# Performance work log

Measured on AMD Instinct MI355X. Metric: run time of the kernel, lower is better.

## Reference

```python
import jax, jax.numpy as jnp
import numpy as np

B, N = 64, 4096          # batch of diagrams, points per diagram
H, W = 64, 64            # persistence-image resolution
L, R = 5, 256            # num_landscapes, landscape resolution
EPS = 1e-8


def setup_inputs() -> dict:
    key = jax.random.key(0)
    k1, = jax.random.split(key, 1)
    u = jax.random.uniform(k1, (B, N, 2), dtype=jnp.float32)
    birth = u[..., 0] * 0.5                      # births in [0, 0.5]
    death = birth + u[..., 1] * 0.5 + 1e-3       # deaths > births, in range
    pairs = jnp.stack([birth, death], axis=-1)   # (B, N, 2)
    sigma = jnp.float32(0.1)                     # learned bandwidth (nn.Parameter)
    return {"pairs": pairs, "sigma": sigma}


def reference(pairs, sigma):
    # ---- Persistence image (batched, vectorized over points) ----
    grid_x = jnp.linspace(0.0, 1.0, W, dtype=pairs.dtype)   # birth axis
    grid_y = jnp.linspace(0.0, 1.0, H, dtype=pairs.dtype)   # persistence axis
    birth = pairs[..., 0]                 # (B, N)
    death = pairs[..., 1]                 # (B, N)
    pers = death - birth                  # (B, N)
    # normalization per config ranges (0,1): divide by (range + 1e-8)
    birth_n = birth / (1.0 + EPS)
    pers_n = pers / (1.0 + EPS)
    weights = pers                        # weight_fn == 'linear'
    inv2s2 = 1.0 / (2.0 * sigma * sigma)
    # separable Gaussian factors: (B, N, W) and (B, N, H)
    gx = jnp.exp(-(grid_x[None, None, :] - birth_n[..., None]) ** 2 * inv2s2)
    gy = jnp.exp(-(grid_y[None, None, :] - pers_n[..., None]) ** 2 * inv2s2)
    # sum_n wt_n * gy_n(h) * gx_n(w)  ->  (B, H, W)
    image = jnp.einsum('bnh,bnw->bhw', gy * weights[..., None], gx)
    image = image / (jnp.max(image, axis=(1, 2), keepdims=True) + EPS)

    # ---- Persistence landscapes ----
    min_b = jnp.min(birth, axis=1, keepdims=True)   # (B, 1)
    max_d = jnp.max(death, axis=1, keepdims=True)   # (B, 1)
    frac = jnp.linspace(0.0, 1.0, R, dtype=pairs.dtype)
    t = min_b + (max_d - min_b) * frac[None, :]     # (B, R)
    rising = jnp.clip(t[:, None, :] - birth[..., None], 0.0)   # (B, N, R)
    falling = jnp.clip(death[..., None] - t[:, None, :], 0.0)  # (B, N, R)
    tents = jnp.minimum(rising, falling)                        # (B, N, R)
    # descending sort over points + take top L == top_k over point axis
    top = jax.lax.top_k(jnp.swapaxes(tents, 1, 2), L)[0]        # (B, R, L)
    landscapes = jnp.swapaxes(top, 1, 2)                        # (B, L, R)
    return image, landscapes
```

## Files before the change

kernel.cpp:

```cpp
#include <hip/hip_runtime.h>
#include <math.h>


#define B_   64
#define N_   4096
#define HW_  64
#define RES_ 256
#define EPSF 1e-8f
#define KC_  8
#define CPB  512
#define LPC_ 8

typedef short short8v  __attribute__((ext_vector_type(8)));
typedef float float4v  __attribute__((ext_vector_type(4)));

__device__ __forceinline__ unsigned pk_bf(float a, float b) {
    unsigned ua = __float_as_uint(a), ub = __float_as_uint(b);
    return ((ua + 0x8000u) >> 16) | ((ub + 0x8000u) & 0xffff0000u);
}

#define INS5(v0, v1, v2, v3, v4, x)                       \
    {                                                     \
        float _p0 = v0, _p1 = v1, _p2 = v2, _p3 = v3;     \
        v0 = fmaxf(_p0, x);                               \
        v1 = __builtin_amdgcn_fmed3f(_p0, _p1, x);        \
        v2 = __builtin_amdgcn_fmed3f(_p1, _p2, x);        \
        v3 = __builtin_amdgcn_fmed3f(_p2, _p3, x);        \
        v4 = __builtin_amdgcn_fmed3f(_p3, v4, x);         \
    }

union SmemU {
    struct {
        unsigned short gy[64 * 72];
        unsigned short gx[64 * 72];
    } img;
    struct {
        float red[8];
    } land;
};

__global__ __launch_bounds__(256) void k_partial(const float* __restrict__ pairs,
                                                 const float* __restrict__ sigp,
                                                 float* __restrict__ part,
                                                 float* __restrict__ lp) {
    __shared__ SmemU sm;
    int tid = threadIdx.x;
    int l = tid & 63;
    int w = __builtin_amdgcn_readfirstlane(tid >> 6);
    int role = blockIdx.x & 1;
    int id   = blockIdx.x >> 1;

    if (role == 0) {
        int kc = id & 7, b = id >> 3;
        float sigma = sigp[0];
        float ncc2 = -(0.5f / (sigma * sigma)) * 1.4426950408889634f;

        int c = tid & 63;
        float xc = (float)c * (1.0f / 63.0f);

        float4v acc[4];
        #pragma unroll
        for (int c4 = 0; c4 < 4; ++c4) acc[c4] = (float4v){0.f, 0.f, 0.f, 0.f};

        int rowA = (w * 16 + (l & 15)) * 72 + (l >> 4) * 8;
        const float4* pb4 = (const float4*)(pairs + 2 * ((size_t)b * N_ + kc * CPB));

        for (int ch = 0; ch < CPB / 64; ++ch) {
            int p0 = ch * 32 + w * 8;
            unsigned gxp[8], gyp[8];
            #pragma unroll
            for (int jp = 0; jp < 8; ++jp) {
                float4 q = pb4[p0 + jp];
                float pe0 = q.y - q.x, pe1 = q.w - q.z;
                float dx0 = xc - q.x, dx1 = xc - q.z;
                float dy0 = xc - pe0, dy1 = xc - pe1;
                float ex0 = __builtin_amdgcn_exp2f(dx0 * dx0 * ncc2);
                float ex1 = __builtin_amdgcn_exp2f(dx1 * dx1 * ncc2);
                float ey0 = pe0 * __builtin_amdgcn_exp2f(dy0 * dy0 * ncc2);
                float ey1 = pe1 * __builtin_amdgcn_exp2f(dy1 * dy1 * ncc2);
                gxp[jp] = pk_bf(ex0, ex1);
                gyp[jp] = pk_bf(ey0, ey1);
            }
            __syncthreads();
            *(uint4*)&sm.img.gy[c * 72 + w * 16]     = *(uint4*)&gyp[0];
            *(uint4*)&sm.img.gy[c * 72 + w * 16 + 8] = *(uint4*)&gyp[4];
            *(uint4*)&sm.img.gx[c * 72 + w * 16]     = *(uint4*)&gxp[0];
            *(uint4*)&sm.img.gx[c * 72 + w * 16 + 8] = *(uint4*)&gxp[4];
            __syncthreads();
            #pragma unroll
            for (int ks = 0; ks < 2; ++ks) {
                short8v af = *(const short8v*)&sm.img.gy[rowA + ks * 32];
                #pragma unroll
                for (int c4 = 0; c4 < 4; ++c4) {
                    short8v bf = *(const short8v*)
                        &sm.img.gx[(c4 * 16 + (l & 15)) * 72 + ks * 32 + (l >> 4) * 8];
                    acc[c4] = __builtin_amdgcn_mfma_f32_16x16x32_bf16(af, bf, acc[c4], 0, 0, 0);
                }
            }
        }

        float* dst = part + (size_t)(b * KC_ + kc) * (HW_ * HW_);
        #pragma unroll
        for (int c4 = 0; c4 < 4; ++c4)
            #pragma unroll
            for (int reg = 0; reg < 4; ++reg) {
                int h = w * 16 + (l >> 4) * 4 + reg;
                int wv = c4 * 16 + (l & 15);
                dst[h * HW_ + wv] = acc[c4][reg];
            }
    } else {
        int pc = id & 7, b = id >> 3;

        const float4* pb4 = (const float4*)(pairs + 2 * (size_t)b * N_);
        float mn = 1e30f, mx = -1e30f;
        #pragma unroll
        for (int i = 0; i < 8; ++i) {
            float4 q = pb4[tid + i * 256];
            mn = fminf(mn, fminf(q.x, q.z));
            mx = fmaxf(mx, fmaxf(q.y, q.w));
        }
        #pragma unroll
        for (int off = 32; off > 0; off >>= 1) {
            mn = fminf(mn, __shfl_xor(mn, off, 64));
            mx = fmaxf(mx, __shfl_xor(mx, off, 64));
        }
        if ((tid & 63) == 0) { sm.land.red[w] = mn; sm.land.red[4 + w] = mx; }
        __syncthreads();
        float minb = fminf(fminf(sm.land.red[0], sm.land.red[1]),
                           fminf(sm.land.red[2], sm.land.red[3]));
        float maxd = fmaxf(fmaxf(sm.land.red[4], sm.land.red[5]),
                           fmaxf(sm.land.red[6], sm.land.red[7]));

        float sc = (maxd - minb) * (1.0f / 255.0f);
        float t  = minb + sc * (float)(w * 64 + l);
        float tlo_f = minb + sc * (float)(w * 64);
        float thi_f = minb + sc * (float)(w * 64 + 63);
        int itlo = __builtin_amdgcn_readfirstlane(__float_as_int(tlo_f));
        int ithi = __builtin_amdgcn_readfirstlane(__float_as_int(thi_f));

        float v0 = 0.f, v1 = 0.f, v2 = 0.f, v3 = 0.f, v4 = 0.f;
        const float4* pw = (const float4*)(pairs + 2 * ((size_t)b * N_ + pc * 512));
        #pragma unroll 2
        for (int p = 0; p < 256; ++p) {
            float4 q = pw[p];
            if (__float_as_int(q.y) > itlo && __float_as_int(q.x) < ithi) {
                float x = fminf(t - q.x, q.y - t);
                INS5(v0, v1, v2, v3, v4, x);
            }
            if (__float_as_int(q.w) > itlo && __float_as_int(q.z) < ithi) {
                float x = fminf(t - q.z, q.w - t);
                INS5(v0, v1, v2, v3, v4, x);
            }
        }

        float* dl = lp + ((size_t)((b * LPC_ + pc) * 4 + w)) * 320;
        dl[0 * 64 + l] = v0;
        dl[1 * 64 + l] = v1;
        dl[2 * 64 + l] = v2;
        dl[3 * 64 + l] = v3;
        dl[4 * 64 + l] = v4;
    }
}

__global__ __launch_bounds__(256) void k_finish(const float* __restrict__ part,
                                                const float* __restrict__ lp,
                                                float* __restrict__ out) {
    __shared__ float redf[4];
    int tid = threadIdx.x;
    if (blockIdx.x < 64) {
        int b = blockIdx.x;
        const float4* p0 = (const float4*)(part + (size_t)b * KC_ * (HW_ * HW_));
        float4 s[4];
        float m = 0.0f;
        #pragma unroll
        for (int i = 0; i < 4; ++i) {
            int pix4 = tid + i * 256;
            float4 v = p0[pix4];
            #pragma unroll
            for (int k2 = 1; k2 < KC_; ++k2) {
                float4 u = p0[(size_t)k2 * 1024 + pix4];
                v.x += u.x; v.y += u.y; v.z += u.z; v.w += u.w;
            }
            s[i] = v;
            m = fmaxf(m, fmaxf(fmaxf(v.x, v.y), fmaxf(v.z, v.w)));
        }
        #pragma unroll
        for (int off = 32; off > 0; off >>= 1) m = fmaxf(m, __shfl_xor(m, off, 64));
        if ((tid & 63) == 0) redf[tid >> 6] = m;
        __syncthreads();
        m = fmaxf(fmaxf(redf[0], redf[1]), fmaxf(redf[2], redf[3]));
        float inv = 1.0f / (m + EPSF);
        float4* od = (float4*)(out + (size_t)b * (HW_ * HW_));
        #pragma unroll
        for (int i = 0; i < 4; ++i) {
            float4 v = s[i];
            v.x *= inv; v.y *= inv; v.z *= inv; v.w *= inv;
            od[tid + i * 256] = v;
        }
    } else {
        int b = blockIdx.x - 64;
        int wq = tid >> 6, l = tid & 63;
        const float* lpb = lp + (size_t)b * (LPC_ * 4 * 320) + wq * 320 + l;
        float u0 = lpb[0 * 64], u1 = lpb[1 * 64], u2 = lpb[2 * 64],
              u3 = lpb[3 * 64], u4 = lpb[4 * 64];
        for (int p2 = 1; p2 < LPC_; ++p2) {
            const float* s2 = lpb + (size_t)p2 * 4 * 320;
            #pragma unroll
            for (int lvl = 0; lvl < 5; ++lvl) {
                float x = s2[lvl * 64];
                INS5(u0, u1, u2, u3, u4, x);
            }
        }
        float* o = out + (size_t)B_ * HW_ * HW_ + (size_t)b * (5 * RES_);
        o[tid]            = u0;
        o[RES_ + tid]     = u1;
        o[2 * RES_ + tid] = u2;
        o[3 * RES_ + tid] = u3;
        o[4 * RES_ + tid] = u4;
    }
}

extern "C" void kernel_launch(void* const* d_in, const int* in_sizes, int n_in,
                              void* d_out, int out_size, void* d_ws, size_t ws_size,
                              hipStream_t stream) {
    const float* pairs = (const float*)d_in[0];
    const float* sig   = (const float*)d_in[1];
    float* out = (float*)d_out;
    float* wsf = (float*)d_ws;

    float* part = wsf;
    float* lp   = part + (size_t)B_ * KC_ * HW_ * HW_;

    k_partial<<<1024, 256, 0, stream>>>(pairs, sig, part, lp);
    k_finish<<<128, 256, 0, stream>>>(part, lp, out);
}
```

Measured before the change: 105.0 us.

## Split partial work finer, precompute min/max in a separate kernel, drop landscape culling branch

Doubles the number of point chunks for both the image and landscape partial sums, giving 2048 blocks instead of 1024. The per-diagram min/max reduction moves out of every landscape block into a small dedicated kernel whose results are read from workspace. The per-point range-culling branch in the landscape insertion loop becomes straight-line code, unrolled by 4, to avoid divergence and branch overhead. The cost is an extra kernel launch, twice as many partial image buffers for the finish kernel to write and reduce, and doing all five median insertions for every point.

```diff
diff --git a/kernel.cpp b/kernel.cpp
--- a/kernel.cpp
+++ b/kernel.cpp
@@ -7,9 +7,9 @@
 #define HW_  64
 #define RES_ 256
 #define EPSF 1e-8f
-#define KC_  8
-#define CPB  512
-#define LPC_ 8
+#define KC_  16
+#define CPB  256
+#define LPC_ 16
 
 typedef short short8v  __attribute__((ext_vector_type(8)));
 typedef float float4v  __attribute__((ext_vector_type(4)));
@@ -39,19 +39,42 @@
     } land;
 };
 
+__global__ __launch_bounds__(256) void k_minmax(const float* __restrict__ pairs,
+                                                float* __restrict__ wsf) {
+    int b = blockIdx.x >> 3, oct = blockIdx.x & 7, tid = threadIdx.x;
+    const float4* pr = (const float4*)(pairs + 2 * ((size_t)b * N_ + oct * 512));
+    float4 q = pr[tid];
+    float mn = fminf(q.x, q.z);
+    float mx = fmaxf(q.y, q.w);
+    #pragma unroll
+    for (int off = 32; off > 0; off >>= 1) {
+        mn = fminf(mn, __shfl_xor(mn, off, 64));
+        mx = fmaxf(mx, __shfl_xor(mx, off, 64));
+    }
+    __shared__ float smn[4], smx[4];
+    if ((tid & 63) == 0) { smn[tid >> 6] = mn; smx[tid >> 6] = mx; }
+    __syncthreads();
+    if (tid == 0) {
+        mn = fminf(fminf(smn[0], smn[1]), fminf(smn[2], smn[3]));
+        mx = fmaxf(fmaxf(smx[0], smx[1]), fmaxf(smx[2], smx[3]));
+        wsf[oct * 64 + b]       = mn;
+        wsf[512 + oct * 64 + b] = mx;
+    }
+}
+
 __global__ __launch_bounds__(256) void k_partial(const float* __restrict__ pairs,
                                                  const float* __restrict__ sigp,
+                                                 const float* __restrict__ wsf,
                                                  float* __restrict__ part,
                                                  float* __restrict__ lp) {
     __shared__ SmemU sm;
     int tid = threadIdx.x;
-    int l = tid & 63;
-    int w = __builtin_amdgcn_readfirstlane(tid >> 6);
+    int l = tid & 63, w = tid >> 6;
     int role = blockIdx.x & 1;
     int id   = blockIdx.x >> 1;
 
     if (role == 0) {
-        int kc = id & 7, b = id >> 3;
+        int kc = id & 15, b = id >> 4;
         float sigma = sigp[0];
         float ncc2 = -(0.5f / (sigma * sigma)) * 1.4426950408889634f;
 
@@ -109,48 +132,27 @@
                 dst[h * HW_ + wv] = acc[c4][reg];
             }
     } else {
-        int pc = id & 7, b = id >> 3;
-
-        const float4* pb4 = (const float4*)(pairs + 2 * (size_t)b * N_);
-        float mn = 1e30f, mx = -1e30f;
-        #pragma unroll
-        for (int i = 0; i < 8; ++i) {
-            float4 q = pb4[tid + i * 256];
-            mn = fminf(mn, fminf(q.x, q.z));
-            mx = fmaxf(mx, fmaxf(q.y, q.w));
-        }
-        #pragma unroll
-        for (int off = 32; off > 0; off >>= 1) {
-            mn = fminf(mn, __shfl_xor(mn, off, 64));
-            mx = fmaxf(mx, __shfl_xor(mx, off, 64));
-        }
-        if ((tid & 63) == 0) { sm.land.red[w] = mn; sm.land.red[4 + w] = mx; }
-        __syncthreads();
-        float minb = fminf(fminf(sm.land.red[0], sm.land.red[1]),
-                           fminf(sm.land.red[2], sm.land.red[3]));
-        float maxd = fmaxf(fmaxf(sm.land.red[4], sm.land.red[5]),
-                           fmaxf(sm.land.red[6], sm.land.red[7]));
+        int pc = id & 15, b = id >> 4;
+
+        float minb = 1e30f, maxd = -1e30f;
+        #pragma unroll
+        for (int oct = 0; oct < 8; ++oct) {
+            minb = fminf(minb, wsf[oct * 64 + b]);
+            maxd = fmaxf(maxd, wsf[512 + oct * 64 + b]);
+        }
 
         float sc = (maxd - minb) * (1.0f / 255.0f);
         float t  = minb + sc * (float)(w * 64 + l);
-        float tlo_f = minb + sc * (float)(w * 64);
-        float thi_f = minb + sc * (float)(w * 64 + 63);
-        int itlo = __builtin_amdgcn_readfirstlane(__float_as_int(tlo_f));
-        int ithi = __builtin_amdgcn_readfirstlane(__float_as_int(thi_f));
 
         float v0 = 0.f, v1 = 0.f, v2 = 0.f, v3 = 0.f, v4 = 0.f;
-        const float4* pw = (const float4*)(pairs + 2 * ((size_t)b * N_ + pc * 512));
-        #pragma unroll 2
-        for (int p = 0; p < 256; ++p) {
+        const float4* pw = (const float4*)(pairs + 2 * ((size_t)b * N_ + pc * CPB));
+        #pragma unroll 4
+        for (int p = 0; p < CPB / 2; ++p) {
             float4 q = pw[p];
-            if (__float_as_int(q.y) > itlo && __float_as_int(q.x) < ithi) {
-                float x = fminf(t - q.x, q.y - t);
-                INS5(v0, v1, v2, v3, v4, x);
-            }
-            if (__float_as_int(q.w) > itlo && __float_as_int(q.z) < ithi) {
-                float x = fminf(t - q.z, q.w - t);
-                INS5(v0, v1, v2, v3, v4, x);
-            }
+            float x0 = fminf(t - q.x, q.y - t);
+            INS5(v0, v1, v2, v3, v4, x0);
+            float x1 = fminf(t - q.z, q.w - t);
+            INS5(v0, v1, v2, v3, v4, x1);
         }
 
         float* dl = lp + ((size_t)((b * LPC_ + pc) * 4 + w)) * 320;
@@ -228,9 +230,10 @@
     float* out = (float*)d_out;
     float* wsf = (float*)d_ws;
 
-    float* part = wsf;
+    float* part = wsf + 1024;
     float* lp   = part + (size_t)B_ * KC_ * HW_ * HW_;
 
-    k_partial<<<1024, 256, 0, stream>>>(pairs, sig, part, lp);
+    k_minmax<<<512, 256, 0, stream>>>(pairs, wsf);
+    k_partial<<<2048, 256, 0, stream>>>(pairs, sig, wsf, part, lp);
     k_finish<<<128, 256, 0, stream>>>(part, lp, out);
 }
```

New measurement: 102.5 us. 2.4% less time.

## Split point chunks finer, stage points in LDS, drop landscape skip test

Applied to the files above, without the earlier changes.

Doubles the number of point chunks per diagram (KC and LPC go from 8 to 16) and launches twice as many blocks. Each chunk's points are staged once into shared memory, where both the image and landscape paths read them. Block roles are interleaved in groups of eight. The landscape loop now drops its per-wave overlap test and inserts every point unconditionally with more unrolling. This trades lower per-block latency and better occupancy for twice the partial-image traffic reduced in the finish kernel, and more insertion work because the branch skip is gone.

```diff
diff --git a/kernel.cpp b/kernel.cpp
--- a/kernel.cpp
+++ b/kernel.cpp
@@ -7,9 +7,9 @@
 #define HW_  64
 #define RES_ 256
 #define EPSF 1e-8f
-#define KC_  8
-#define CPB  512
-#define LPC_ 8
+#define KC_  16
+#define CPB  256
+#define LPC_ 16
 
 typedef short short8v  __attribute__((ext_vector_type(8)));
 typedef float float4v  __attribute__((ext_vector_type(4)));
@@ -30,13 +30,8 @@
     }
 
 union SmemU {
-    struct {
-        unsigned short gy[64 * 72];
-        unsigned short gx[64 * 72];
-    } img;
-    struct {
-        float red[8];
-    } land;
+    struct { unsigned short gy[64 * 72]; unsigned short gx[64 * 72]; } img;
+    struct { float red[8]; } land;
 };
 
 __global__ __launch_bounds__(256) void k_partial(const float* __restrict__ pairs,
@@ -44,14 +39,19 @@
                                                  float* __restrict__ part,
                                                  float* __restrict__ lp) {
     __shared__ SmemU sm;
+    __shared__ float4 ptsS[128];
     int tid = threadIdx.x;
-    int l = tid & 63;
-    int w = __builtin_amdgcn_readfirstlane(tid >> 6);
-    int role = blockIdx.x & 1;
-    int id   = blockIdx.x >> 1;
+    int l = tid & 63, w = tid >> 6;
+    unsigned g = blockIdx.x;
+    int role = (g >> 3) & 1;
+    int id   = (int)(((g >> 4) << 3) | (g & 7));
+
+    int sub = id & 15, b = id >> 4;
+
+    const float4* src = (const float4*)(pairs + 2 * ((size_t)b * N_ + sub * CPB));
+    if (tid < 128) ptsS[tid] = src[tid];
 
     if (role == 0) {
-        int kc = id & 7, b = id >> 3;
         float sigma = sigp[0];
         float ncc2 = -(0.5f / (sigma * sigma)) * 1.4426950408889634f;
 
@@ -63,14 +63,14 @@
         for (int c4 = 0; c4 < 4; ++c4) acc[c4] = (float4v){0.f, 0.f, 0.f, 0.f};
 
         int rowA = (w * 16 + (l & 15)) * 72 + (l >> 4) * 8;
-        const float4* pb4 = (const float4*)(pairs + 2 * ((size_t)b * N_ + kc * CPB));
+        __syncthreads();
 
         for (int ch = 0; ch < CPB / 64; ++ch) {
             int p0 = ch * 32 + w * 8;
             unsigned gxp[8], gyp[8];
             #pragma unroll
             for (int jp = 0; jp < 8; ++jp) {
-                float4 q = pb4[p0 + jp];
+                float4 q = ptsS[p0 + jp];
                 float pe0 = q.y - q.x, pe1 = q.w - q.z;
                 float dx0 = xc - q.x, dx1 = xc - q.z;
                 float dy0 = xc - pe0, dy1 = xc - pe1;
@@ -99,7 +99,7 @@
             }
         }
 
-        float* dst = part + (size_t)(b * KC_ + kc) * (HW_ * HW_);
+        float* dst = part + (size_t)(b * KC_ + sub) * (HW_ * HW_);
         #pragma unroll
         for (int c4 = 0; c4 < 4; ++c4)
             #pragma unroll
@@ -109,8 +109,6 @@
                 dst[h * HW_ + wv] = acc[c4][reg];
             }
     } else {
-        int pc = id & 7, b = id >> 3;
-
         const float4* pb4 = (const float4*)(pairs + 2 * (size_t)b * N_);
         float mn = 1e30f, mx = -1e30f;
         #pragma unroll
@@ -133,27 +131,18 @@
 
         float sc = (maxd - minb) * (1.0f / 255.0f);
         float t  = minb + sc * (float)(w * 64 + l);
-        float tlo_f = minb + sc * (float)(w * 64);
-        float thi_f = minb + sc * (float)(w * 64 + 63);
-        int itlo = __builtin_amdgcn_readfirstlane(__float_as_int(tlo_f));
-        int ithi = __builtin_amdgcn_readfirstlane(__float_as_int(thi_f));
 
         float v0 = 0.f, v1 = 0.f, v2 = 0.f, v3 = 0.f, v4 = 0.f;
-        const float4* pw = (const float4*)(pairs + 2 * ((size_t)b * N_ + pc * 512));
-        #pragma unroll 2
-        for (int p = 0; p < 256; ++p) {
-            float4 q = pw[p];
-            if (__float_as_int(q.y) > itlo && __float_as_int(q.x) < ithi) {
-                float x = fminf(t - q.x, q.y - t);
-                INS5(v0, v1, v2, v3, v4, x);
-            }
-            if (__float_as_int(q.w) > itlo && __float_as_int(q.z) < ithi) {
-                float x = fminf(t - q.z, q.w - t);
-                INS5(v0, v1, v2, v3, v4, x);
-            }
-        }
-
-        float* dl = lp + ((size_t)((b * LPC_ + pc) * 4 + w)) * 320;
+        #pragma unroll 4
+        for (int p = 0; p < CPB / 2; ++p) {
+            float4 q = ptsS[p];
+            float x0 = fminf(t - q.x, q.y - t);
+            INS5(v0, v1, v2, v3, v4, x0);
+            float x1 = fminf(t - q.z, q.w - t);
+            INS5(v0, v1, v2, v3, v4, x1);
+        }
+
+        float* dl = lp + ((size_t)((b * LPC_ + sub) * 4 + w)) * 320;
         dl[0 * 64 + l] = v0;
         dl[1 * 64 + l] = v1;
         dl[2 * 64 + l] = v2;
@@ -231,6 +220,6 @@
     float* part = wsf;
     float* lp   = part + (size_t)B_ * KC_ * HW_ * HW_;
 
-    k_partial<<<1024, 256, 0, stream>>>(pairs, sig, part, lp);
+    k_partial<<<2048, 256, 0, stream>>>(pairs, sig, part, lp);
     k_finish<<<128, 256, 0, stream>>>(part, lp, out);
 }
```

Result: faster. 99.11 us (-5.6%).
